# Kernel optimization log

Hardware: AMD Instinct MI355X
Metric: run time of the kernel (lower is better)

## Reference

```python
import jax, jax.numpy as jnp
import numpy as np

K = 8
D_IN = 300 + K   # 308
H = 100          # hidden size hardcoded throughout the module
N = 768          # num_words (words in one table)


def setup_inputs() -> dict:
    key = jax.random.key(0)
    ks = jax.random.split(key, 24)
    f32 = jnp.float32

    def rn(k, shape, scale=0.05):
        return jax.random.normal(k, shape, dtype=f32) * scale

    inp = {
        'vv': jax.random.normal(ks[0], (N, D_IN), dtype=f32),
        'indices': jax.random.randint(ks[1], (N, 5), 0, N),
        'indices_not_found': jax.random.randint(ks[2], (N,), 0, 2).astype(bool),
        'num_words': N,
        # ModuleA: Linear(308, 100) + tanh
        'A_W': rn(ks[3], (D_IN, H)), 'A_b': jnp.zeros((H,), f32),
        # ModuleB: consumes concat(ww[N,500], hh[N,100]) -> Linear(600,100)+tanh
        'B_W': rn(ks[4], (5 * H + H, H)), 'B_b': jnp.zeros((H,), f32),
        # ModuleB2(100,100,100): two heads, oo and new hidden hh
        'B2_Wo': rn(ks[5], (H, H)), 'B2_bo': jnp.zeros((H,), f32),
        'B2_Wh': rn(ks[6], (H, H)), 'B2_bh': jnp.zeros((H,), f32),
        # ModuleD(100,100)
        'D_W': rn(ks[7], (H, H)), 'D_b': jnp.zeros((H,), f32),
    }
    # Three ModuleAssociate2 heads (rows/cols/cells): pairwise 2-layer MLP
    # score(o_i, o_j) = Linear(H,2)(relu(Linear(2H,H)(concat(o_i,o_j))))
    for i, name in enumerate(['rows', 'cols', 'cells']):
        k1, k2 = jax.random.split(ks[8 + i])
        inp[name + '_W1'] = rn(k1, (2 * H, H))
        inp[name + '_b1'] = jnp.zeros((H,), f32)
        inp[name + '_W2'] = rn(k2, (H, 2))
        inp[name + '_b2'] = jnp.zeros((2,), f32)
    return inp


def _concat_neighbors(uu, indices, not_found):
    # gather 5 neighbor feature rows -> (N, 5*H); zero rows where not found
    y = uu[indices].reshape(indices.shape[0], 5 * uu.shape[1])  # (N,5,H)->(N,500)
    return jnp.where(not_found[:, None], 0.0, y)


def _associate(o, W1, b1, W2, b2):
    # pairwise MLP over all (i,j) pairs without materializing the 2H concat:
    # concat(o_i,o_j) @ W1 == o_i @ W1[:H] + o_j @ W1[H:]
    h = o.shape[1]
    hl = o @ W1[:h]   # (N,H)
    hr = o @ W1[h:]   # (N,H)
    hid = jax.nn.relu(hl[:, None, :] + hr[None, :, :] + b1)  # (N,N,H)
    return hid @ W2 + b2  # (N,N,2)


def reference(indices, indices_not_found, vv, num_words,
              A_W, A_b, B_W, B_b, B2_Wo, B2_bo, B2_Wh, B2_bh, D_W, D_b,
              rows_W1, rows_b1, rows_W2, rows_b2,
              cols_W1, cols_b1, cols_W2, cols_b2,
              cells_W1, cells_b1, cells_W2, cells_b2):
    iterations = 1
    uu = jnp.tanh(vv @ A_W + A_b)                 # ModuleA: (N,100)
    hh = jnp.zeros((num_words, H), vv.dtype)
    for _ in range(iterations):
        ww = _concat_neighbors(uu, indices, indices_not_found)  # (N,500)
        bb = jnp.tanh(jnp.concatenate([ww, hh], axis=1) @ B_W + B_b)  # ModuleB
        oo = jnp.tanh(bb @ B2_Wo + B2_bo)          # ModuleB2 output head
        hh = jnp.tanh(bb @ B2_Wh + B2_bh)          # ModuleB2 hidden head
        uu = jnp.tanh(hh @ D_W + D_b)              # ModuleD
    return (_associate(oo, rows_W1, rows_b1, rows_W2, rows_b2),
            _associate(oo, cols_W1, cols_b1, cols_W2, cols_b2),
            _associate(oo, cells_W1, cells_b1, cells_W2, cells_b2))
```

## Files before the change

kernel.cpp:

```cpp
#include <hip/hip_runtime.h>
#include <hip/hip_bf16.h>

#define NW   768
#define HID  100
#define DIN  308
#define RPB  2

typedef const float* fp;

__global__ __launch_bounds__(192) void k_probe(const int* __restrict__ nf,
                                               const int* __restrict__ idx,
                                               int* __restrict__ modes) {
    __shared__ int bigNF, badNF, oddNF, evenNF, oddIX, evenIX;
    if (threadIdx.x == 0) { bigNF = badNF = oddNF = evenNF = oddIX = evenIX = 0; }
    __syncthreads();
    const int t = threadIdx.x;
    const unsigned vn = (unsigned)nf[t];
    if (vn > 1u) atomicOr(&bigNF, 1);
    if (vn & 0xFEFEFEFEu) atomicOr(&badNF, 1);
    if ((t & 1) && vn) atomicOr(&oddNF, 1);
    if (!(t & 1) && vn) atomicOr(&evenNF, 1);
    const unsigned vi = (unsigned)idx[t];
    if ((t & 1) && vi) atomicOr(&oddIX, 1);
    if (!(t & 1) && vi) atomicOr(&evenIX, 1);
    __syncthreads();
    if (t == 0) {
        int m = 0;
        if (!badNF && bigNF) m = 1;
        else if (!oddNF && evenNF) m = 2;
        modes[0] = m;
        modes[1] = (!oddIX && evenIX) ? 1 : 0;
    }
}

__global__ __launch_bounds__(512) void k_uu(fp vv, fp A_W, fp A_b,
                                            float* __restrict__ uu) {
    __shared__ float vs[RPB][DIN];
    __shared__ float part[4][RPB][128];
    const int i0 = blockIdx.x * RPB;
    for (int t = threadIdx.x; t < RPB * DIN; t += 512) {
        const int r = t / DIN, k = t % DIN;
        vs[r][k] = vv[(i0 + r) * DIN + k];
    }
    __syncthreads();
    const int c = threadIdx.x & 127;
    const int s = threadIdx.x >> 7;
    float a0 = 0.f, a1 = 0.f;
    if (c < HID) {
        const int k0 = s * 77;
#pragma unroll 11
        for (int k = k0; k < k0 + 77; ++k) {
            const float w = A_W[k * HID + c];
            a0 = fmaf(vs[0][k], w, a0);
            a1 = fmaf(vs[1][k], w, a1);
        }
    }
    part[s][0][c] = a0; part[s][1][c] = a1;
    __syncthreads();
    for (int t = threadIdx.x; t < RPB * HID; t += 512) {
        const int r = t / HID, cc = t % HID;
        float acc = A_b[cc];
#pragma unroll
        for (int s2 = 0; s2 < 4; ++s2) acc += part[s2][r][cc];
        uu[(i0 + r) * HID + cc] = tanhf(acc);
    }
}

__global__ __launch_bounds__(640) void k_fused(
    const float* __restrict__ uu, const int* __restrict__ indices,
    const int* __restrict__ nf, const int* __restrict__ modes,
    fp B_W, fp B_b, fp B2_Wo, fp B2_bo,
    fp W1r, fp b1r, fp W1c, fp b1c, fp W1e, fp b1e,
    float* __restrict__ hlhr) {
    __shared__ float ww[RPB][5 * HID];
    __shared__ float part[5][RPB][128];
    __shared__ float bbs[RPB][HID];
    __shared__ float oos[RPB][HID];
    const int i0 = blockIdx.x * RPB;
    const int mnf = modes[0], midx = modes[1];

    for (int t = threadIdx.x; t < RPB * 5 * HID; t += 640) {
        const int r = t / (5 * HID), u = t % (5 * HID);
        const int i = i0 + r;
        const bool notf = (mnf == 1) ? (((const unsigned char*)nf)[i] != 0)
                        : (mnf == 2) ? (nf[2 * i] != 0)
                                     : (nf[i] != 0);
        const int q = u / HID, cc = u % HID;
        int j = midx ? indices[2 * (i * 5 + q)] : indices[i * 5 + q];
        j = (j < 0) ? 0 : ((j >= NW) ? NW - 1 : j);
        ww[r][u] = notf ? 0.f : uu[j * HID + cc];
    }
    __syncthreads();

    const int c = threadIdx.x % 128;
    const int s = threadIdx.x / 128;

    {
        float a0 = 0.f, a1 = 0.f;
        if (c < HID) {
            const int k0 = s * 100;
#pragma unroll 10
            for (int k = k0; k < k0 + 100; ++k) {
                const float w = B_W[k * HID + c];
                a0 = fmaf(ww[0][k], w, a0);
                a1 = fmaf(ww[1][k], w, a1);
            }
        }
        part[s][0][c] = a0; part[s][1][c] = a1;
    }
    __syncthreads();
    for (int t = threadIdx.x; t < RPB * HID; t += 640) {
        const int r = t / HID, cc = t % HID;
        float acc = B_b[cc];
#pragma unroll
        for (int s2 = 0; s2 < 5; ++s2) acc += part[s2][r][cc];
        bbs[r][cc] = tanhf(acc);
    }
    __syncthreads();

    {
        float a0 = 0.f, a1 = 0.f;
        if (c < HID) {
            const int k0 = s * 20;
#pragma unroll 10
            for (int k = k0; k < k0 + 20; ++k) {
                const float w = B2_Wo[k * HID + c];
                a0 = fmaf(bbs[0][k], w, a0);
                a1 = fmaf(bbs[1][k], w, a1);
            }
        }
        part[s][0][c] = a0; part[s][1][c] = a1;
    }
    __syncthreads();
    for (int t = threadIdx.x; t < RPB * HID; t += 640) {
        const int r = t / HID, cc = t % HID;
        float acc = B2_bo[cc];
#pragma unroll
        for (int s2 = 0; s2 < 5; ++s2) acc += part[s2][r][cc];
        oos[r][cc] = tanhf(acc);
    }
    __syncthreads();

    const int u = threadIdx.x;
    if (u < 600) {
        const int ho = u / HID;
        const int cc = u % HID;
        const int h = ho >> 1, half = ho & 1;
        fp W1 = (h == 0) ? W1r : ((h == 1) ? W1c : W1e);
        fp b1 = (h == 0) ? b1r : ((h == 1) ? b1c : b1e);
        const float bias = half ? 0.f : b1[cc];
        float a0 = bias, a1 = bias;
        const float* Wp = W1 + half * HID * HID;
#pragma unroll 10
        for (int k = 0; k < HID; ++k) {
            const float w = Wp[k * HID + cc];
            a0 = fmaf(oos[0][k], w, a0);
            a1 = fmaf(oos[1][k], w, a1);
        }
        hlhr[(size_t)ho * (NW * HID) + (size_t)(i0 + 0) * HID + cc] = a0;
        hlhr[(size_t)ho * (NW * HID) + (size_t)(i0 + 1) * HID + cc] = a1;
    }
}

__device__ __forceinline__ int swzi(int r, int c) {
    return r * 128 + (c ^ (((r >> 1) & 7) << 2));
}

__global__ __launch_bounds__(256) void k_pair(
    const float* __restrict__ hlhr,
    fp W2r, fp b2r, fp W2c, fp b2c, fp W2e, fp b2e,
    float* __restrict__ out) {
    __shared__ __align__(16) float hlT[32 * 128];
    __shared__ __align__(16) float hrT[32 * 128];
    __shared__ __align__(16) float w2a[HID];
    __shared__ __align__(16) float w2b[HID];

    const int h  = blockIdx.z;
    const int i0 = blockIdx.y * 32;
    const int j0 = blockIdx.x * 32;
    const float* hl = hlhr + (size_t)(h * 2 + 0) * (NW * HID) + i0 * HID;
    const float* hr = hlhr + (size_t)(h * 2 + 1) * (NW * HID) + j0 * HID;

    for (int t = threadIdx.x; t < 32 * HID; t += 256) {
        const int r = t / HID, c = t % HID;
        hlT[swzi(r, c)] = hl[t];
        hrT[swzi(r, c)] = hr[t];
    }
    fp W2 = (h == 0) ? W2r : ((h == 1) ? W2c : W2e);
    fp b2 = (h == 0) ? b2r : ((h == 1) ? b2c : b2e);
    if (threadIdx.x < HID) {
        w2a[threadIdx.x] = W2[threadIdx.x * 2 + 0];
        w2b[threadIdx.x] = W2[threadIdx.x * 2 + 1];
    }
    __syncthreads();

    const int tx = threadIdx.x & 15;
    const int ty = threadIdx.x >> 4;
    float acc[2][2][2] = {};

#pragma unroll
    for (int k = 0; k < HID; k += 4) {
        const float4 a0 = *(const float4*)&hlT[swzi(ty * 2 + 0, k)];
        const float4 a1 = *(const float4*)&hlT[swzi(ty * 2 + 1, k)];
        const float4 r0 = *(const float4*)&hrT[swzi(tx * 2 + 0, k)];
        const float4 r1 = *(const float4*)&hrT[swzi(tx * 2 + 1, k)];
        const float4 wa = *(const float4*)&w2a[k];
        const float4 wb = *(const float4*)&w2b[k];
#define STEP(cmp)                                                              \
        {                                                                      \
            const float h00 = fmaxf(a0.cmp + r0.cmp, 0.f);                     \
            const float h01 = fmaxf(a0.cmp + r1.cmp, 0.f);                     \
            const float h10 = fmaxf(a1.cmp + r0.cmp, 0.f);                     \
            const float h11 = fmaxf(a1.cmp + r1.cmp, 0.f);                     \
            acc[0][0][0] = fmaf(h00, wa.cmp, acc[0][0][0]);                    \
            acc[0][0][1] = fmaf(h00, wb.cmp, acc[0][0][1]);                    \
            acc[0][1][0] = fmaf(h01, wa.cmp, acc[0][1][0]);                    \
            acc[0][1][1] = fmaf(h01, wb.cmp, acc[0][1][1]);                    \
            acc[1][0][0] = fmaf(h10, wa.cmp, acc[1][0][0]);                    \
            acc[1][0][1] = fmaf(h10, wb.cmp, acc[1][0][1]);                    \
            acc[1][1][0] = fmaf(h11, wa.cmp, acc[1][1][0]);                    \
            acc[1][1][1] = fmaf(h11, wb.cmp, acc[1][1][1]);                    \
        }
        STEP(x) STEP(y) STEP(z) STEP(w)
#undef STEP
    }

    const float b20 = b2[0];
    const float b21 = b2[1];
#pragma unroll
    for (int ii = 0; ii < 2; ++ii)
#pragma unroll
        for (int jj = 0; jj < 2; ++jj) {
            const int i = i0 + ty * 2 + ii;
            const int j = j0 + tx * 2 + jj;
            const size_t o = ((size_t)(h * NW + i) * NW + j) * 2;
            float2 v;
            v.x = acc[ii][jj][0] + b20;
            v.y = acc[ii][jj][1] + b21;
            *reinterpret_cast<float2*>(out + o) = v;
        }
}

extern "C" void kernel_launch(void* const* d_in, const int* in_sizes, int n_in,
                              void* d_out, int out_size, void* d_ws,
                              size_t ws_size, hipStream_t stream) {
    int i_vv = -1, i_idx = -1, i_nf = -1, i_AW = -1, i_BW = -1;
    int tens[3] = {-1, -1, -1}; int n10 = 0;
    int w1s[3]  = {-1, -1, -1}; int n20 = 0;
    int w2s[3]  = {-1, -1, -1}; int n200 = 0;
    int b100[8] = {-1, -1, -1, -1, -1, -1, -1, -1}; int nb = 0;
    int b2s[3]  = {-1, -1, -1}; int nb2 = 0;
    for (int i = 0; i < n_in; ++i) {
        switch (in_sizes[i]) {
            case 236544: i_vv = i; break;
            case 3840:   i_idx = i; break;
            case 768:    i_nf = i; break;
            case 30800:  i_AW = i; break;
            case 60000:  i_BW = i; break;
            case 10000:  if (n10 < 3) tens[n10++] = i; break;
            case 20000:  if (n20 < 3) w1s[n20++] = i; break;
            case 200:    if (n200 < 3) w2s[n200++] = i; break;
            case 100:    if (nb < 8) b100[nb++] = i; break;
            case 2:      if (nb2 < 3) b2s[nb2++] = i; break;
            default: break;
        }
    }
    fp vv          = (fp)d_in[i_vv];
    const int* idx = (const int*)d_in[i_idx];
    const int* nf  = (const int*)d_in[i_nf];
    fp A_W = (fp)d_in[i_AW],      A_b   = (fp)d_in[b100[0]];
    fp B_W = (fp)d_in[i_BW],      B_b   = (fp)d_in[b100[1]];
    fp B2_Wo = (fp)d_in[tens[0]], B2_bo = (fp)d_in[b100[2]];
    fp W1r = (fp)d_in[w1s[0]], b1r = (fp)d_in[b100[5]];
    fp W1c = (fp)d_in[w1s[1]], b1c = (fp)d_in[b100[6]];
    fp W1e = (fp)d_in[w1s[2]], b1e = (fp)d_in[b100[7]];
    fp W2r = (fp)d_in[w2s[0]], b2r = (fp)d_in[b2s[0]];
    fp W2c = (fp)d_in[w2s[1]], b2c = (fp)d_in[b2s[1]];
    fp W2e = (fp)d_in[w2s[2]], b2e = (fp)d_in[b2s[2]];

    float* out = (float*)d_out;

    float* ws    = (float*)d_ws;
    float* uu    = ws;
    float* hlhr  = ws + NW * HID;
    int*   modes = (int*)(ws + NW * HID + 6 * NW * HID);

    k_probe<<<1, 192, 0, stream>>>(nf, idx, modes);
    k_uu<<<NW / RPB, 512, 0, stream>>>(vv, A_W, A_b, uu);
    k_fused<<<NW / RPB, 640, 0, stream>>>(uu, idx, nf, modes, B_W, B_b,
                                          B2_Wo, B2_bo,
                                          W1r, b1r, W1c, b1c, W1e, b1e, hlhr);
    dim3 grid(NW / 32, NW / 32, 3);
    k_pair<<<grid, 256, 0, stream>>>(hlhr, W2r, b2r, W2c, b2c, W2e, b2e, out);
}
```

Before: 54.71 us.

## Transpose hl/hr to k-major layout and enlarge pairwise tile to 64x64 with 4x4 micro-tiles

The fused kernel now writes hl/hr transposed (hidden index major, word index minor) using float2 stores. The pairwise kernel loads 64x64 tiles with coalesced k-major reads and computes a 4x4 block of pairs per thread, so each shared-memory load is reused across more pairs. Output is written as float4. This cuts the grid to a quarter as many blocks, which may lower occupancy, and raises register pressure from the 32 accumulators per thread.

```diff
diff --git a/kernel.cpp b/kernel.cpp
--- a/kernel.cpp
+++ b/kernel.cpp
@@ -5,6 +5,7 @@
 #define HID  100
 #define DIN  308
 #define RPB  2
+#define TJ   64
 
 typedef const float* fp;
 
@@ -71,7 +72,7 @@
     const int* __restrict__ nf, const int* __restrict__ modes,
     fp B_W, fp B_b, fp B2_Wo, fp B2_bo,
     fp W1r, fp b1r, fp W1c, fp b1c, fp W1e, fp b1e,
-    float* __restrict__ hlhr) {
+    float* __restrict__ hlhrT) {
     __shared__ float ww[RPB][5 * HID];
     __shared__ float part[5][RPB][128];
     __shared__ float bbs[RPB][HID];
@@ -157,34 +158,31 @@
             a0 = fmaf(oos[0][k], w, a0);
             a1 = fmaf(oos[1][k], w, a1);
         }
-        hlhr[(size_t)ho * (NW * HID) + (size_t)(i0 + 0) * HID + cc] = a0;
-        hlhr[(size_t)ho * (NW * HID) + (size_t)(i0 + 1) * HID + cc] = a1;
-    }
-}
-
-__device__ __forceinline__ int swzi(int r, int c) {
-    return r * 128 + (c ^ (((r >> 1) & 7) << 2));
+        float2 v; v.x = a0; v.y = a1;
+        *reinterpret_cast<float2*>(
+            &hlhrT[(size_t)ho * (HID * NW) + (size_t)cc * NW + i0]) = v;
+    }
 }
 
 __global__ __launch_bounds__(256) void k_pair(
-    const float* __restrict__ hlhr,
+    const float* __restrict__ hlhrT,
     fp W2r, fp b2r, fp W2c, fp b2c, fp W2e, fp b2e,
     float* __restrict__ out) {
-    __shared__ __align__(16) float hlT[32 * 128];
-    __shared__ __align__(16) float hrT[32 * 128];
+    __shared__ __align__(16) float hlS[HID][TJ];
+    __shared__ __align__(16) float hrS[HID][TJ];
     __shared__ __align__(16) float w2a[HID];
     __shared__ __align__(16) float w2b[HID];
 
     const int h  = blockIdx.z;
-    const int i0 = blockIdx.y * 32;
-    const int j0 = blockIdx.x * 32;
-    const float* hl = hlhr + (size_t)(h * 2 + 0) * (NW * HID) + i0 * HID;
-    const float* hr = hlhr + (size_t)(h * 2 + 1) * (NW * HID) + j0 * HID;
-
-    for (int t = threadIdx.x; t < 32 * HID; t += 256) {
-        const int r = t / HID, c = t % HID;
-        hlT[swzi(r, c)] = hl[t];
-        hrT[swzi(r, c)] = hr[t];
+    const int i0 = blockIdx.y * TJ;
+    const int j0 = blockIdx.x * TJ;
+    const float* hlg = hlhrT + (size_t)(h * 2 + 0) * (HID * NW);
+    const float* hrg = hlhrT + (size_t)(h * 2 + 1) * (HID * NW);
+
+    for (int t = threadIdx.x; t < HID * TJ; t += 256) {
+        const int k = t / TJ, j = t % TJ;
+        hlS[k][j] = hlg[k * NW + i0 + j];
+        hrS[k][j] = hrg[k * NW + j0 + j];
     }
     fp W2 = (h == 0) ? W2r : ((h == 1) ? W2c : W2e);
     fp b2 = (h == 0) ? b2r : ((h == 1) ? b2c : b2e);
@@ -196,49 +194,46 @@
 
     const int tx = threadIdx.x & 15;
     const int ty = threadIdx.x >> 4;
-    float acc[2][2][2] = {};
-
-#pragma unroll
-    for (int k = 0; k < HID; k += 4) {
-        const float4 a0 = *(const float4*)&hlT[swzi(ty * 2 + 0, k)];
-        const float4 a1 = *(const float4*)&hlT[swzi(ty * 2 + 1, k)];
-        const float4 r0 = *(const float4*)&hrT[swzi(tx * 2 + 0, k)];
-        const float4 r1 = *(const float4*)&hrT[swzi(tx * 2 + 1, k)];
-        const float4 wa = *(const float4*)&w2a[k];
-        const float4 wb = *(const float4*)&w2b[k];
-#define STEP(cmp)                                                              \
-        {                                                                      \
-            const float h00 = fmaxf(a0.cmp + r0.cmp, 0.f);                     \
-            const float h01 = fmaxf(a0.cmp + r1.cmp, 0.f);                     \
-            const float h10 = fmaxf(a1.cmp + r0.cmp, 0.f);                     \
-            const float h11 = fmaxf(a1.cmp + r1.cmp, 0.f);                     \
-            acc[0][0][0] = fmaf(h00, wa.cmp, acc[0][0][0]);                    \
-            acc[0][0][1] = fmaf(h00, wb.cmp, acc[0][0][1]);                    \
-            acc[0][1][0] = fmaf(h01, wa.cmp, acc[0][1][0]);                    \
-            acc[0][1][1] = fmaf(h01, wb.cmp, acc[0][1][1]);                    \
-            acc[1][0][0] = fmaf(h10, wa.cmp, acc[1][0][0]);                    \
-            acc[1][0][1] = fmaf(h10, wb.cmp, acc[1][0][1]);                    \
-            acc[1][1][0] = fmaf(h11, wa.cmp, acc[1][1][0]);                    \
-            acc[1][1][1] = fmaf(h11, wb.cmp, acc[1][1][1]);                    \
-        }
-        STEP(x) STEP(y) STEP(z) STEP(w)
-#undef STEP
+    float acc[4][4][2] = {};
+
+    for (int kb = 0; kb < HID; kb += 4) {
+        const float4 wa4 = *(const float4*)&w2a[kb];
+        const float4 wb4 = *(const float4*)&w2b[kb];
+        const float wav[4] = {wa4.x, wa4.y, wa4.z, wa4.w};
+        const float wbv[4] = {wb4.x, wb4.y, wb4.z, wb4.w};
+#pragma unroll
+        for (int q = 0; q < 4; ++q) {
+            const int k = kb + q;
+            const float4 a4 = *(const float4*)&hlS[k][ty * 4];
+            const float4 r4 = *(const float4*)&hrS[k][tx * 4];
+            const float av[4] = {a4.x, a4.y, a4.z, a4.w};
+            const float rv[4] = {r4.x, r4.y, r4.z, r4.w};
+            const float wa = wav[q], wb = wbv[q];
+#pragma unroll
+            for (int ii = 0; ii < 4; ++ii)
+#pragma unroll
+                for (int jj = 0; jj < 4; ++jj) {
+                    const float hv = fmaxf(av[ii] + rv[jj], 0.f);
+                    acc[ii][jj][0] = fmaf(hv, wa, acc[ii][jj][0]);
+                    acc[ii][jj][1] = fmaf(hv, wb, acc[ii][jj][1]);
+                }
+        }
     }
 
     const float b20 = b2[0];
     const float b21 = b2[1];
 #pragma unroll
-    for (int ii = 0; ii < 2; ++ii)
-#pragma unroll
-        for (int jj = 0; jj < 2; ++jj) {
-            const int i = i0 + ty * 2 + ii;
-            const int j = j0 + tx * 2 + jj;
-            const size_t o = ((size_t)(h * NW + i) * NW + j) * 2;
-            float2 v;
-            v.x = acc[ii][jj][0] + b20;
-            v.y = acc[ii][jj][1] + b21;
-            *reinterpret_cast<float2*>(out + o) = v;
-        }
+    for (int ii = 0; ii < 4; ++ii) {
+        const int i = i0 + ty * 4 + ii;
+        const size_t rowo = ((size_t)(h * NW + i) * NW + j0 + tx * 4) * 2;
+        float4 v0, v1;
+        v0.x = acc[ii][0][0] + b20; v0.y = acc[ii][0][1] + b21;
+        v0.z = acc[ii][1][0] + b20; v0.w = acc[ii][1][1] + b21;
+        v1.x = acc[ii][2][0] + b20; v1.y = acc[ii][2][1] + b21;
+        v1.z = acc[ii][3][0] + b20; v1.w = acc[ii][3][1] + b21;
+        *reinterpret_cast<float4*>(out + rowo)     = v0;
+        *reinterpret_cast<float4*>(out + rowo + 4) = v1;
+    }
 }
 
 extern "C" void kernel_launch(void* const* d_in, const int* in_sizes, int n_in,
@@ -282,14 +277,14 @@
 
     float* ws    = (float*)d_ws;
     float* uu    = ws;
-    float* hlhr  = ws + NW * HID;
+    float* hlhrT = ws + NW * HID;
     int*   modes = (int*)(ws + NW * HID + 6 * NW * HID);
 
     k_probe<<<1, 192, 0, stream>>>(nf, idx, modes);
     k_uu<<<NW / RPB, 512, 0, stream>>>(vv, A_W, A_b, uu);
     k_fused<<<NW / RPB, 640, 0, stream>>>(uu, idx, nf, modes, B_W, B_b,
                                           B2_Wo, B2_bo,
-                                          W1r, b1r, W1c, b1c, W1e, b1e, hlhr);
-    dim3 grid(NW / 32, NW / 32, 3);
-    k_pair<<<grid, 256, 0, stream>>>(hlhr, W2r, b2r, W2c, b2c, W2e, b2e, out);
-}
+                                          W1r, b1r, W1c, b1c, W1e, b1e, hlhrT);
+    dim3 grid(NW / TJ, NW / TJ, 3);
+    k_pair<<<grid, 256, 0, stream>>>(hlhrT, W2r, b2r, W2c, b2c, W2e, b2e, out);
+}
```

Measured after the change: 61.62 us. 12.6% more time.
